# Kernel tuning notes

Measured on AMD Instinct MI355X. Metric: run time of the kernel, lower is better.

Reference implementation:

```python
import jax, jax.numpy as jnp
import numpy as np

IMG = 800.0
OUT = 7          # output_size
SR = 2           # sampling_ratio
SCALES = (0.25, 0.125, 0.0625, 0.03125)  # FPN strides 4,8,16,32
CANON_SCALE = 224.0
CANON_LVL = 4.0
K_MIN, K_MAX = 2.0, 5.0  # -log2(scales[0]), -log2(scales[-1])
EPS = 1e-6


def setup_inputs() -> dict:
    key = jax.random.key(0)
    k0, k1, k2, k3, kp = jax.random.split(key, 5)
    feat0 = jax.random.normal(k0, (2, 256, 200, 200), dtype=jnp.float32)
    feat1 = jax.random.normal(k1, (2, 256, 100, 100), dtype=jnp.float32)
    feat2 = jax.random.normal(k2, (2, 256, 50, 50), dtype=jnp.float32)
    feat3 = jax.random.normal(k3, (2, 256, 25, 25), dtype=jnp.float32)
    # two random corner points per box, sorted so x0<=x1, y0<=y1
    pts = jax.random.uniform(kp, (2, 512, 2, 2), dtype=jnp.float32) * IMG
    proposals = jnp.concatenate([pts.min(axis=2), pts.max(axis=2)], axis=-1)  # [B,N,4] = x0,y0,x1,y1
    return {"feat0": feat0, "feat1": feat1, "feat2": feat2, "feat3": feat3,
            "proposals": proposals}


def _roi_align(feat, bidx, boxes, scale):
    """torchvision roi_align (aligned=False) for all boxes on one feature map.
    feat: [B,C,H,W], bidx: [N] int32 image index, boxes: [N,4] image coords.
    Returns [N,C,OUT,OUT]."""
    H, W = feat.shape[2], feat.shape[3]
    x0 = boxes[:, 0] * scale
    y0 = boxes[:, 1] * scale
    x1 = boxes[:, 2] * scale
    y1 = boxes[:, 3] * scale
    roi_w = jnp.maximum(x1 - x0, 1.0)
    roi_h = jnp.maximum(y1 - y0, 1.0)
    bin_w = roi_w / OUT
    bin_h = roi_h / OUT
    # sample offsets within the roi, in bin units: [OUT*SR]
    off = (jnp.arange(OUT, dtype=jnp.float32)[:, None]
           + (jnp.arange(SR, dtype=jnp.float32)[None, :] + 0.5) / SR).reshape(-1)
    ys = y0[:, None] + off[None, :] * bin_h[:, None]  # [N, OUT*SR]
    xs = x0[:, None] + off[None, :] * bin_w[:, None]  # [N, OUT*SR]

    def prep(c, size):
        valid = (c >= -1.0) & (c <= float(size))
        cc = jnp.maximum(c, 0.0)
        lo0 = jnp.floor(cc).astype(jnp.int32)
        at_edge = lo0 >= size - 1
        lo = jnp.where(at_edge, size - 1, lo0)
        hi = jnp.where(at_edge, size - 1, lo0 + 1)
        frac = jnp.where(at_edge, 0.0, cc - lo0.astype(cc.dtype))
        return lo, hi, frac, valid

    yl, yh, ly, vy = prep(ys, H)
    xl, xh, lx, vx = prep(xs, W)
    hy, hx = 1.0 - ly, 1.0 - lx
    b3 = bidx[:, None, None]

    def gather(yi, xi):
        # advanced indices (b, y, x) with channel slice -> [N, Sy, Sx, C]
        return feat[b3, :, yi[:, :, None], xi[:, None, :]]

    val = ((hy[:, :, None] * hx[:, None, :])[..., None] * gather(yl, xl)
           + (hy[:, :, None] * lx[:, None, :])[..., None] * gather(yl, xh)
           + (ly[:, :, None] * hx[:, None, :])[..., None] * gather(yh, xl)
           + (ly[:, :, None] * lx[:, None, :])[..., None] * gather(yh, xh))
    mask = (vy[:, :, None] & vx[:, None, :]).astype(val.dtype)[..., None]
    val = val * mask
    N, C = boxes.shape[0], feat.shape[1]
    val = val.reshape(N, OUT, SR, OUT, SR, C).mean(axis=(2, 4))  # avg over samples
    return val.transpose(0, 3, 1, 2)  # [N, C, OUT, OUT]


def reference(feat0, feat1, feat2, feat3, proposals):
    feats = (feat0, feat1, feat2, feat3)
    B, Np = proposals.shape[0], proposals.shape[1]
    boxes = proposals.reshape(-1, 4)                      # [N,4]
    bidx = jnp.repeat(jnp.arange(B, dtype=jnp.int32), Np)  # image id per roi
    # LevelMapper: FPN paper heuristic
    areas = (boxes[:, 2] - boxes[:, 0]) * (boxes[:, 3] - boxes[:, 1])
    s = jnp.sqrt(areas)
    lvls = jnp.floor(CANON_LVL + jnp.log2(s / CANON_SCALE + EPS))
    lvls = (jnp.clip(lvls, K_MIN, K_MAX) - K_MIN).astype(jnp.int32)  # 0..3
    N, C = boxes.shape[0], feat0.shape[1]
    result = jnp.zeros((N, C, OUT, OUT), dtype=feat0.dtype)
    for l, (feat, scale) in enumerate(zip(feats, SCALES)):
        pooled = _roi_align(feat, bidx, boxes, scale)
        result = result + jnp.where((lvls == l)[:, None, None, None], pooled, 0.0)
    return result
```

## Files before the change

### kernel.cpp

```cpp
#include <hip/hip_runtime.h>
#include <hip/hip_fp16.h>
#include <math.h>

#define POUT 7
#define NCH 256

#define HW0 40000
#define HW1 10000
#define HW2 2500
#define HW3 625
#define WS_OFF0 0
#define WS_OFF1 (2*NCH*HW0)
#define WS_OFF2 (WS_OFF1 + 2*NCH*HW1)
#define WS_OFF3 (WS_OFF2 + 2*NCH*HW2)
#define WS_ELEMS (WS_OFF3 + 2*NCH*HW3)
#define WS_NEED  ((size_t)(WS_ELEMS + 256) * sizeof(float))

#define TP 112
#define TC 128
#define TSTR 113
#define NT0 ((HW0 + TP - 1) / TP)
#define NT1 ((HW1 + TP - 1) / TP)
#define NT2 ((HW2 + TP - 1) / TP)
#define NT3 ((HW3 + TP - 1) / TP)

__global__ __launch_bounds__(512) void transpose_fused_kernel(
    const float* __restrict__ f0, const float* __restrict__ f1,
    const float* __restrict__ f2, const float* __restrict__ f3,
    float* __restrict__ ws, int B)
{
    __shared__ float tile[TC * TSTR];

    int id = blockIdx.x;
    const int s0 = NT0 * 2 * B, s1 = NT1 * 2 * B, s2 = NT2 * 2 * B;
    const float* src; int HW, nt; size_t woff;
    if (id < s0)                 { src = f0; HW = HW0; nt = NT0; woff = WS_OFF0; }
    else if (id - s0 < s1)       { id -= s0; src = f1; HW = HW1; nt = NT1; woff = WS_OFF1; }
    else if (id - s0 - s1 < s2)  { id -= s0 + s1; src = f2; HW = HW2; nt = NT2; woff = WS_OFF2; }
    else                         { id -= s0 + s1 + s2; src = f3; HW = HW3; nt = NT3; woff = WS_OFF3; }

    const int tl   = id % nt;
    const int rest = id / nt;
    const int ch   = rest & 1;
    const int bb   = rest >> 1;
    const int p0   = tl * TP;
    const int c0   = ch * TC;
    const int pn   = min(TP, HW - p0);

    const int t = threadIdx.x;
    const float* sbase = src + ((size_t)(bb * NCH + c0)) * HW + p0;

    const int nf4 = TC * (TP / 4);
    if (pn == TP) {
        for (int i = t; i < nf4; i += 512) {
            const int c  = i / (TP / 4);
            const int p4 = i - c * (TP / 4);
            const float4 v = *(const float4*)&sbase[(size_t)c * HW + p4 * 4];
            float* d = &tile[c * TSTR + p4 * 4];
            d[0] = v.x; d[1] = v.y; d[2] = v.z; d[3] = v.w;
        }
    } else {
        for (int i = t; i < nf4; i += 512) {
            const int c  = i / (TP / 4);
            const int pb = (i - c * (TP / 4)) * 4;
            float v[4] = {0.f, 0.f, 0.f, 0.f};
            for (int k = 0; k < 4; ++k)
                if (pb + k < pn) v[k] = sbase[(size_t)c * HW + pb + k];
            float* d = &tile[c * TSTR + pb];
            d[0] = v[0]; d[1] = v[1]; d[2] = v[2]; d[3] = v[3];
        }
    }
    __syncthreads();

    float* dbase = ws + woff + ((size_t)bb * HW + p0) * NCH + c0;
    const int nf2 = (TC / 2) * TP;
    for (int i = t; i < nf2; i += 512) {
        const int p  = i >> 6;
        const int c2 = i & 63;
        if (p < pn) {
            float2 w;
            w.x = tile[(2 * c2    ) * TSTR + p];
            w.y = tile[(2 * c2 + 1) * TSTR + p];
            *(float2*)&dbase[(size_t)p * NCH + 2 * c2] = w;
        }
    }
}

__global__ __launch_bounds__(256, 4) void roi_gather_kernel(
    const float* __restrict__ ws, const float* __restrict__ props,
    float* __restrict__ out, int boxes_per_img)
{
    __shared__ int4  sRec[196];
    __shared__ float sStage[64 * 49];

    const int n = blockIdx.x;
    const int t = threadIdx.x;
    const int b = n / boxes_per_img;

    const float4 box = ((const float4*)props)[n];
    const float area = (box.z - box.x) * (box.w - box.y);
    float lvlf = floorf(4.0f + log2f(sqrtf(area) / 224.0f + 1e-6f));
    lvlf = fminf(fmaxf(lvlf, 2.0f), 5.0f) - 2.0f;
    const int l = (int)lvlf;

    int sz; size_t lvl_off;
    if      (l == 0) { sz = 200; lvl_off = WS_OFF0; }
    else if (l == 1) { sz = 100; lvl_off = WS_OFF1; }
    else if (l == 2) { sz = 50;  lvl_off = WS_OFF2; }
    else             { sz = 25;  lvl_off = WS_OFF3; }
    const int HW = sz * sz;
    const float scale = 0.25f / (float)(1 << l);

    if (t < 196) {
        const int bin = t >> 2, sub = t & 3;
        const int ph = bin / POUT, pw = bin % POUT;
        const int iy = sub >> 1,  ix = sub & 1;

        const float x0 = box.x * scale, y0 = box.y * scale;
        const float x1 = box.z * scale, y1 = box.w * scale;
        const float bin_w = fmaxf(x1 - x0, 1.0f) / (float)POUT;
        const float bin_h = fmaxf(y1 - y0, 1.0f) / (float)POUT;

        const float ys = y0 + ((float)ph + ((float)iy + 0.5f) * 0.5f) * bin_h;
        const float xs = x0 + ((float)pw + ((float)ix + 0.5f) * 0.5f) * bin_w;

        const bool  vy  = (ys >= -1.0f) && (ys <= (float)sz);
        const float cy  = fmaxf(ys, 0.0f);
        const int   yl0 = (int)floorf(cy);
        const bool  ey  = yl0 >= sz - 1;
        const int   yl  = ey ? sz - 1 : yl0;
        const int   yh  = ey ? sz - 1 : yl0 + 1;
        const float ly  = ey ? 0.0f : cy - (float)yl0;

        const bool  vx  = (xs >= -1.0f) && (xs <= (float)sz);
        const float cx  = fmaxf(xs, 0.0f);
        const int   xl0 = (int)floorf(cx);
        const bool  ex  = xl0 >= sz - 1;
        const int   xl  = ex ? sz - 1 : xl0;
        const float lx  = ex ? 0.0f : cx - (float)xl0;

        const float hy = 1.0f - ly, hx = 1.0f - lx;
        const float m  = (vy && vx) ? 0.25f : 0.0f;
        const float w00 = hy * hx * m, w01 = hy * lx * m;
        const float w10 = ly * hx * m, w11 = ly * lx * m;

        __half2 p01 = __floats2half2_rn(w00, w01);
        __half2 p23 = __floats2half2_rn(w10, w11);

        int4 rec;
        rec.x = (yl * sz + xl) * NCH;
        rec.y = *reinterpret_cast<const int*>(&p01);
        rec.z = *reinterpret_cast<const int*>(&p23);
        rec.w = (yh * sz + xl) * NCH;
        sRec[t] = rec;
    }
    __syncthreads();

    const float* fb = ws + lvl_off + (size_t)b * (size_t)HW * NCH + t;

    float acc[49];
    #pragma unroll
    for (int bin = 0; bin < 49; ++bin) {
        float a = 0.0f;
        #pragma unroll
        for (int sub = 0; sub < 4; ++sub) {
            const int4 rec = sRec[bin * 4 + sub];
            const __half2 h01 = *reinterpret_cast<const __half2*>(&rec.y);
            const __half2 h23 = *reinterpret_cast<const __half2*>(&rec.z);
            const float2 w01 = __half22float2(h01);
            const float2 w23 = __half22float2(h23);
            a += w01.x * fb[rec.x] + w01.y * fb[rec.x + NCH]
               + w23.x * fb[rec.w] + w23.y * fb[rec.w + NCH];
        }
        acc[bin] = a;
    }

    __syncthreads();
    float* obase = out + (size_t)n * (NCH * 49);
    #pragma unroll
    for (int r = 0; r < 4; ++r) {
        if ((t >> 6) == r) {
            #pragma unroll
            for (int i = 0; i < 49; ++i) sStage[(t & 63) * 49 + i] = acc[i];
        }
        __syncthreads();
        float4* d4 = (float4*)(obase + r * (64 * 49));
        const float4* s4 = (const float4*)sStage;
        for (int i = t; i < 64 * 49 / 4; i += 256) d4[i] = s4[i];
        __syncthreads();
    }
}

__global__ __launch_bounds__(256, 4) void roi_align_nchw_kernel(
    const float* __restrict__ f0, const float* __restrict__ f1,
    const float* __restrict__ f2, const float* __restrict__ f3,
    const float* __restrict__ props, float* __restrict__ out, int boxes_per_img)
{
    const int n = blockIdx.x;
    const int t = threadIdx.x;
    if (t >= 196) return;
    const int bin = t >> 2, q = t & 3;
    const int ph = bin / POUT, pw = bin % POUT;
    const int iy = q >> 1,    ix = q & 1;
    const int b = n / boxes_per_img;

    const float4 box = ((const float4*)props)[n];
    const float area = (box.z - box.x) * (box.w - box.y);
    float lvlf = floorf(4.0f + log2f(sqrtf(area) / 224.0f + 1e-6f));
    lvlf = fminf(fmaxf(lvlf, 2.0f), 5.0f) - 2.0f;
    const int l = (int)lvlf;

    const float* feat; int sz;
    if      (l == 0) { feat = f0; sz = 200; }
    else if (l == 1) { feat = f1; sz = 100; }
    else if (l == 2) { feat = f2; sz = 50;  }
    else             { feat = f3; sz = 25;  }
    const float scale = 0.25f / (float)(1 << l);

    const float x0 = box.x * scale, y0 = box.y * scale;
    const float x1 = box.z * scale, y1 = box.w * scale;
    const float bin_w = fmaxf(x1 - x0, 1.0f) / (float)POUT;
    const float bin_h = fmaxf(y1 - y0, 1.0f) / (float)POUT;
    const float ysamp = y0 + ((float)ph + ((float)iy + 0.5f) * 0.5f) * bin_h;
    const float xsamp = x0 + ((float)pw + ((float)ix + 0.5f) * 0.5f) * bin_w;

    const bool  vy  = (ysamp >= -1.0f) && (ysamp <= (float)sz);
    const float cy  = fmaxf(ysamp, 0.0f);
    const int   yl0 = (int)floorf(cy);
    const bool  ey  = yl0 >= sz - 1;
    const int   yl  = ey ? sz - 1 : yl0;
    const int   yh  = ey ? sz - 1 : yl0 + 1;
    const float ly  = ey ? 0.0f : cy - (float)yl0;
    const bool  vx  = (xsamp >= -1.0f) && (xsamp <= (float)sz);
    const float cx  = fmaxf(xsamp, 0.0f);
    const int   xl0 = (int)floorf(cx);
    const bool  ex  = xl0 >= sz - 1;
    const int   xl  = ex ? sz - 1 : xl0;
    const int   xh  = ex ? sz - 1 : xl0 + 1;
    const float lx  = ex ? 0.0f : cx - (float)xl0;

    const float hy = 1.0f - ly, hx = 1.0f - lx;
    const float m  = (vy && vx) ? 1.0f : 0.0f;
    const float w00 = hy * hx * m, w01 = hy * lx * m;
    const float w10 = ly * hx * m, w11 = ly * lx * m;

    const int HW = sz * sz;
    const float* base = feat + (size_t)b * NCH * HW;
    int o00 = yl * sz + xl, o01 = yl * sz + xh;
    int o10 = yh * sz + xl, o11 = yh * sz + xh;
    float* op = out + (size_t)n * NCH * (POUT * POUT) + bin;

    #pragma unroll 4
    for (int cch = 0; cch < NCH; ++cch) {
        float v = w00 * base[o00] + w01 * base[o01]
                + w10 * base[o10] + w11 * base[o11];
        v += __shfl_xor(v, 1);
        v += __shfl_xor(v, 2);
        if (q == 0) op[cch * (POUT * POUT)] = v * 0.25f;
        o00 += HW; o01 += HW; o10 += HW; o11 += HW;
    }
}

extern "C" void kernel_launch(void* const* d_in, const int* in_sizes, int n_in,
                              void* d_out, int out_size, void* d_ws, size_t ws_size,
                              hipStream_t stream) {
    const float* f0 = (const float*)d_in[0];
    const float* f1 = (const float*)d_in[1];
    const float* f2 = (const float*)d_in[2];
    const float* f3 = (const float*)d_in[3];
    const float* props = (const float*)d_in[4];
    float* out = (float*)d_out;

    const int N = in_sizes[4] / 4;
    const int B = in_sizes[0] / (NCH * HW0);
    const int boxes_per_img = N / B;

    if (ws_size >= WS_NEED && B == 2) {
        float* wsf = (float*)d_ws;
        hipMemsetAsync(wsf + WS_ELEMS, 0, 256 * sizeof(float), stream);
        const int nblk = (NT0 + NT1 + NT2 + NT3) * 2 * B;
        transpose_fused_kernel<<<nblk, 512, 0, stream>>>(f0, f1, f2, f3, wsf, B);
        roi_gather_kernel<<<N, 256, 0, stream>>>(wsf, props, out, boxes_per_img);
    } else {
        roi_align_nchw_kernel<<<N, 256, 0, stream>>>(f0, f1, f2, f3, props, out, boxes_per_img);
    }
}
```

Baseline: 233.1 us.

## Sort ROIs by image/level/center for locality; shrink transpose tiles; fold memset

Block 0 of the transpose kernel now computes a spatial sort key per box (image, FPN level, center y/x) and bitonic-sorts all 1024 boxes in shared memory, writing a permutation that the gather kernel uses to process boxes in a locality-friendly, XCD-interleaved order. The transpose tile shrinks to 56 pixels with a channel-pair interleaved LDS layout so the write-out reads float2 directly, and the launch bound requests higher occupancy. The separate memset is folded into the transpose kernel, removing one launch. The sort adds serial work on a single block, and the fast path is now restricted to N == 1024.

```diff
diff --git a/kernel.cpp b/kernel.cpp
--- a/kernel.cpp
+++ b/kernel.cpp
@@ -14,75 +14,105 @@
 #define WS_OFF2 (WS_OFF1 + 2*NCH*HW1)
 #define WS_OFF3 (WS_OFF2 + 2*NCH*HW2)
 #define WS_ELEMS (WS_OFF3 + 2*NCH*HW3)
-#define WS_NEED  ((size_t)(WS_ELEMS + 256) * sizeof(float))
-
-#define TP 112
-#define TC 128
-#define TSTR 113
+#define WS_PERM_OFF (WS_ELEMS + 256)
+#define WS_NEED  ((size_t)(WS_PERM_OFF + 1024) * sizeof(float))
+
+#define TP 56
+#define RS 114
 #define NT0 ((HW0 + TP - 1) / TP)
 #define NT1 ((HW1 + TP - 1) / TP)
 #define NT2 ((HW2 + TP - 1) / TP)
 #define NT3 ((HW3 + TP - 1) / TP)
-
-__global__ __launch_bounds__(512) void transpose_fused_kernel(
+#define NBLK ((NT0 + NT1 + NT2 + NT3) * 4)
+
+__global__ __launch_bounds__(512, 8) void transpose_fused_kernel(
     const float* __restrict__ f0, const float* __restrict__ f1,
     const float* __restrict__ f2, const float* __restrict__ f3,
-    float* __restrict__ ws, int B)
+    float* __restrict__ ws, const float* __restrict__ props,
+    int boxes_per_img, int N)
 {
-    __shared__ float tile[TC * TSTR];
-
-    int id = blockIdx.x;
-    const int s0 = NT0 * 2 * B, s1 = NT1 * 2 * B, s2 = NT2 * 2 * B;
+    __shared__ float tile[64 * RS];
+
+    const int gid = blockIdx.x;
+    int id = gid;
     const float* src; int HW, nt; size_t woff;
-    if (id < s0)                 { src = f0; HW = HW0; nt = NT0; woff = WS_OFF0; }
-    else if (id - s0 < s1)       { id -= s0; src = f1; HW = HW1; nt = NT1; woff = WS_OFF1; }
-    else if (id - s0 - s1 < s2)  { id -= s0 + s1; src = f2; HW = HW2; nt = NT2; woff = WS_OFF2; }
-    else                         { id -= s0 + s1 + s2; src = f3; HW = HW3; nt = NT3; woff = WS_OFF3; }
-
-    const int tl   = id % nt;
-    const int rest = id / nt;
-    const int ch   = rest & 1;
-    const int bb   = rest >> 1;
-    const int p0   = tl * TP;
-    const int c0   = ch * TC;
-    const int pn   = min(TP, HW - p0);
-
-    const int t = threadIdx.x;
+    if (id < NT0 * 4)                        { src = f0; HW = HW0; nt = NT0; woff = WS_OFF0; }
+    else if ((id -= NT0 * 4) < NT1 * 4)      { src = f1; HW = HW1; nt = NT1; woff = WS_OFF1; }
+    else if ((id -= NT1 * 4) < NT2 * 4)      { src = f2; HW = HW2; nt = NT2; woff = WS_OFF2; }
+    else { id -= NT2 * 4;                      src = f3; HW = HW3; nt = NT3; woff = WS_OFF3; }
+
+    const int ch = id & 1;
+    const int tl = (id >> 1) % nt;
+    const int bb = (id >> 1) / nt;
+    const int p0 = tl * TP;
+    const int pn = min(TP, HW - p0);
+    const int c0 = ch * 128;
+    const int t  = threadIdx.x;
+
     const float* sbase = src + ((size_t)(bb * NCH + c0)) * HW + p0;
 
-    const int nf4 = TC * (TP / 4);
     if (pn == TP) {
-        for (int i = t; i < nf4; i += 512) {
+        for (int i = t; i < 128 * (TP / 4); i += 512) {
             const int c  = i / (TP / 4);
             const int p4 = i - c * (TP / 4);
             const float4 v = *(const float4*)&sbase[(size_t)c * HW + p4 * 4];
-            float* d = &tile[c * TSTR + p4 * 4];
-            d[0] = v.x; d[1] = v.y; d[2] = v.z; d[3] = v.w;
+            float* d = &tile[(c >> 1) * RS + (c & 1) + p4 * 8];
+            d[0] = v.x; d[2] = v.y; d[4] = v.z; d[6] = v.w;
         }
     } else {
-        for (int i = t; i < nf4; i += 512) {
+        for (int i = t; i < 128 * (TP / 4); i += 512) {
             const int c  = i / (TP / 4);
             const int pb = (i - c * (TP / 4)) * 4;
-            float v[4] = {0.f, 0.f, 0.f, 0.f};
+            float vv[4];
+            #pragma unroll
             for (int k = 0; k < 4; ++k)
-                if (pb + k < pn) v[k] = sbase[(size_t)c * HW + pb + k];
-            float* d = &tile[c * TSTR + pb];
-            d[0] = v[0]; d[1] = v[1]; d[2] = v[2]; d[3] = v[3];
+                vv[k] = (pb + k < pn) ? sbase[(size_t)c * HW + pb + k] : 0.0f;
+            float* d = &tile[(c >> 1) * RS + (c & 1) + pb * 2];
+            d[0] = vv[0]; d[2] = vv[1]; d[4] = vv[2]; d[6] = vv[3];
         }
     }
     __syncthreads();
 
     float* dbase = ws + woff + ((size_t)bb * HW + p0) * NCH + c0;
-    const int nf2 = (TC / 2) * TP;
-    for (int i = t; i < nf2; i += 512) {
-        const int p  = i >> 6;
-        const int c2 = i & 63;
+    for (int i = t; i < 64 * TP; i += 512) {
+        const int c2 = i & 63, p = i >> 6;
         if (p < pn) {
-            float2 w;
-            w.x = tile[(2 * c2    ) * TSTR + p];
-            w.y = tile[(2 * c2 + 1) * TSTR + p];
-            *(float2*)&dbase[(size_t)p * NCH + 2 * c2] = w;
-        }
+            const float2 v = *(const float2*)&tile[c2 * RS + 2 * p];
+            *(float2*)&dbase[(size_t)p * NCH + 2 * c2] = v;
+        }
+    }
+
+    if (gid == 0) {
+        __syncthreads();
+        unsigned* keys = (unsigned*)tile;
+        if (N == 1024) {
+            for (int i = t; i < 1024; i += 512) {
+                const float4 box = ((const float4*)props)[i];
+                const float area = (box.z - box.x) * (box.w - box.y);
+                float lvlf = floorf(4.0f + log2f(sqrtf(area) / 224.0f + 1e-6f));
+                lvlf = fminf(fmaxf(lvlf, 2.0f), 5.0f) - 2.0f;
+                const int l = (int)lvlf;
+                const float sc = 0.25f / (float)(1 << l);
+                int yc = (int)(0.5f * (box.y + box.w) * sc);
+                int xc = (int)(0.5f * (box.x + box.z) * sc);
+                yc = yc < 0 ? 0 : (yc > 255 ? 255 : yc);
+                xc = xc < 0 ? 0 : (xc > 255 ? 255 : xc);
+                const unsigned hi = (unsigned)((i / boxes_per_img) * 4 + l);
+                keys[i] = (((hi << 8 | (unsigned)yc) << 8 | (unsigned)xc) << 10) | (unsigned)i;
+            }
+            for (int size = 2; size <= 1024; size <<= 1)
+                for (int stride = size >> 1; stride > 0; stride >>= 1) {
+                    __syncthreads();
+                    const int lo = t & (stride - 1);
+                    const int k  = ((t ^ lo) << 1) | lo;
+                    const unsigned a = keys[k], b2 = keys[k + stride];
+                    if ((a > b2) == ((k & size) == 0)) { keys[k] = b2; keys[k + stride] = a; }
+                }
+            __syncthreads();
+            int* perm = (int*)(ws + WS_PERM_OFF);
+            for (int i = t; i < 1024; i += 512) perm[i] = (int)(keys[i] & 1023u);
+        }
+        if (t < 256) ws[WS_ELEMS + t] = 0.0f;
     }
 }
 
@@ -93,7 +123,8 @@
     __shared__ int4  sRec[196];
     __shared__ float sStage[64 * 49];
 
-    const int n = blockIdx.x;
+    const int* perm = (const int*)(ws + WS_PERM_OFF);
+    const int n = perm[(blockIdx.x & 7) * 128 + (blockIdx.x >> 3)];
     const int t = threadIdx.x;
     const int b = n / boxes_per_img;
 
@@ -275,11 +306,10 @@
     const int B = in_sizes[0] / (NCH * HW0);
     const int boxes_per_img = N / B;
 
-    if (ws_size >= WS_NEED && B == 2) {
+    if (ws_size >= WS_NEED && B == 2 && N == 1024) {
         float* wsf = (float*)d_ws;
-        hipMemsetAsync(wsf + WS_ELEMS, 0, 256 * sizeof(float), stream);
-        const int nblk = (NT0 + NT1 + NT2 + NT3) * 2 * B;
-        transpose_fused_kernel<<<nblk, 512, 0, stream>>>(f0, f1, f2, f3, wsf, B);
+        transpose_fused_kernel<<<NBLK, 512, 0, stream>>>(f0, f1, f2, f3, wsf,
+                                                         props, boxes_per_img, N);
         roi_gather_kernel<<<N, 256, 0, stream>>>(wsf, props, out, boxes_per_img);
     } else {
         roi_align_nchw_kernel<<<N, 256, 0, stream>>>(f0, f1, f2, f3, props, out, boxes_per_img);
```

New measurement: 223.5 us. 1.04x faster.
